# Optimization experiments

Measured on AMD Instinct MI355X. Metric: run time of the kernel, lower is better.

Reference implementation:

```python
import jax, jax.numpy as jnp
import numpy as np

N = 100000        # nodes
E = 1600000       # edges (avg degree 16)
IN, HID, OUT = 128, 128, 40
K = 3             # Chebyshev order
NUM_HID = 5       # hidden ChebConv layers between first and last


def setup_inputs() -> dict:
    key = jax.random.key(0)
    ks = jax.random.split(key, 8)
    s = 0.05
    return dict(
        features=jax.random.normal(ks[0], (N, IN), jnp.float32),
        src=jax.random.randint(ks[1], (E,), 0, N),
        dst=jax.random.randint(ks[2], (E,), 0, N),
        W0=jax.random.normal(ks[3], (K * IN, HID), jnp.float32) * s,
        b0=jnp.zeros((HID,), jnp.float32),
        Wh=jax.random.normal(ks[4], (NUM_HID, K * HID, HID), jnp.float32) * s,
        bh=jnp.zeros((NUM_HID, HID), jnp.float32),
        Wl=jax.random.normal(ks[5], (K * HID, OUT), jnp.float32) * s,
        bl=jnp.zeros((OUT,), jnp.float32),
    )


def _cheb_conv(X, src, dst, dinv, W, b):
    """One DGL ChebConv with lambda_max=2 (re_norm=1): relu(cat(X_0..X_{K-1}) @ W + b)."""
    def spmm(Y):  # A_hat @ Y = D^-1/2 A D^-1/2 Y via gather/segment-sum
        msg = (Y * dinv)[src]                                  # [E, d]
        return jax.ops.segment_sum(msg, dst, num_segments=N) * dinv

    X0 = X
    bases = [X0]
    X1 = -spmm(X0)                       # X_1 = -A_hat X  (re_norm - 1 == 0)
    bases.append(X1)
    for _ in range(2, K):
        X2 = -2.0 * spmm(X1) - X0        # X_t = -2 A_hat X_{t-1} - X_{t-2}
        bases.append(X2)
        X0, X1 = X1, X2
    Xt = jnp.concatenate(bases, axis=1)  # [N, K*d]
    return jax.nn.relu(Xt @ W + b)


def reference(features, src, dst, W0, b0, Wh, bh, Wl, bl):
    # symmetric normalization from in-degrees (clamped at 1), as in DGL ChebConv
    deg = jax.ops.segment_sum(jnp.ones((E,), jnp.float32), dst, num_segments=N)
    dinv = jnp.clip(deg, 1.0, None) ** -0.5
    dinv = dinv[:, None]                 # [N, 1]

    h = _cheb_conv(features, src, dst, dinv, W0, b0)
    for i in range(NUM_HID):             # dropout is identity in eval mode
        h = _cheb_conv(h, src, dst, dinv, Wh[i], bh[i])
    return _cheb_conv(h, src, dst, dinv, Wl, bl)
```

## Files before the change

### kernel.cpp

```cpp
#include <hip/hip_runtime.h>
#include <hip/hip_bf16.h>


#define NN 100000
#define EE 1600000
#define FF 128
#define NBK 1563
#define EPB 4096
#define CAP 3072

typedef __attribute__((ext_vector_type(8))) short short8_t;
typedef __attribute__((ext_vector_type(8))) _Float16 half8_t;
typedef __attribute__((ext_vector_type(4))) _Float16 half4_t;
typedef __attribute__((ext_vector_type(4))) float floatx4;
typedef __attribute__((ext_vector_type(4))) float accfrag;


__global__ __launch_bounds__(256) void bhist_kernel(const int* __restrict__ dst,
                                                    int* __restrict__ bcnt) {
    __shared__ int lh[NBK];
    int tid = threadIdx.x;
    for (int j = tid; j < NBK; j += 256) lh[j] = 0;
    __syncthreads();
    int e0 = blockIdx.x * EPB;
#pragma unroll
    for (int k = 0; k < EPB / 256; ++k) {
        int i = e0 + k * 256 + tid;
        if (i < EE) atomicAdd(&lh[dst[i] >> 6], 1);
    }
    __syncthreads();
    for (int j = tid; j < NBK; j += 256)
        if (lh[j] > 0) atomicAdd(&bcnt[j], lh[j]);
}

__global__ __launch_bounds__(256) void scan_p1_kernel(const int* __restrict__ cnt,
                                                      int* __restrict__ bsum, int n) {
    __shared__ int red[8];
    int i = blockIdx.x * 256 + threadIdx.x;
    int v = (i < n) ? cnt[i] : 0;
    for (int off = 32; off > 0; off >>= 1) v += __shfl_down(v, off, 64);
    int wv = threadIdx.x >> 6;
    if ((threadIdx.x & 63) == 0) red[wv] = v;
    __syncthreads();
    if (threadIdx.x == 0) bsum[blockIdx.x] = red[0] + red[1] + red[2] + red[3];
}

__global__ __launch_bounds__(1024) void scan_p2_kernel(int* __restrict__ bsum, int nb) {
    __shared__ int s[1024];
    int tid = threadIdx.x;
    int v = (tid < nb) ? bsum[tid] : 0;
    s[tid] = v;
    __syncthreads();
    for (int off = 1; off < 1024; off <<= 1) {
        int u = (tid >= off) ? s[tid - off] : 0;
        __syncthreads();
        s[tid] += u;
        __syncthreads();
    }
    if (tid < nb) bsum[tid] = s[tid] - v;
}

__global__ __launch_bounds__(256) void scan_p3_kernel(const int* __restrict__ cnt,
                                                      const int* __restrict__ bsum,
                                                      int* __restrict__ out_ptr, int n) {
    __shared__ int s[256];
    int tid = threadIdx.x;
    int i = blockIdx.x * 256 + tid;
    int v = (i < n) ? cnt[i] : 0;
    s[tid] = v;
    __syncthreads();
    for (int off = 1; off < 256; off <<= 1) {
        int u = (tid >= off) ? s[tid - off] : 0;
        __syncthreads();
        s[tid] += u;
        __syncthreads();
    }
    if (i < n) {
        int excl = bsum[blockIdx.x] + s[tid] - v;
        out_ptr[i] = excl;
        if (i == n - 1) out_ptr[n] = excl + v;
    }
}

__global__ __launch_bounds__(256) void bscatter_kernel(
    const int* __restrict__ src, const int* __restrict__ dst,
    const int* __restrict__ bptr, int* __restrict__ bfill, int* __restrict__ ebuf) {
    __shared__ int lh[NBK];
    __shared__ int lbase[NBK];
    int tid = threadIdx.x;
    for (int j = tid; j < NBK; j += 256) lh[j] = 0;
    __syncthreads();
    int e0 = blockIdx.x * EPB;
#pragma unroll
    for (int k = 0; k < EPB / 256; ++k) {
        int i = e0 + k * 256 + tid;
        if (i < EE) atomicAdd(&lh[dst[i] >> 6], 1);
    }
    __syncthreads();
    for (int j = tid; j < NBK; j += 256)
        if (lh[j] > 0) lbase[j] = atomicAdd(&bfill[j], lh[j]);
    __syncthreads();
    for (int j = tid; j < NBK; j += 256) lh[j] = 0;
    __syncthreads();
#pragma unroll
    for (int k = 0; k < EPB / 256; ++k) {
        int i = e0 + k * 256 + tid;
        if (i < EE) {
            int d = dst[i];
            int b = d >> 6;
            int off = atomicAdd(&lh[b], 1);
            ebuf[bptr[b] + lbase[b] + off] = (src[i] << 6) | (d & 63);
        }
    }
}

__global__ __launch_bounds__(256) void csr_build_kernel(
    const int* __restrict__ ebuf, const int* __restrict__ bptr,
    int* __restrict__ rowptr, int* __restrict__ colsrc,
    float* __restrict__ dinv, float* __restrict__ dinv2, float* __restrict__ sdeg) {
    __shared__ int pk[CAP];
    __shared__ int ob[CAP];
    __shared__ int cnt[64];
    __shared__ int sexcl[64];
    __shared__ int fill[64];

    int tid = threadIdx.x;
    int b = blockIdx.x;
    int start = bptr[b];
    int cb = bptr[b + 1] - start;
    if (cb > CAP) cb = CAP;

    if (tid < 64) { cnt[tid] = 0; fill[tid] = 0; }
    __syncthreads();

    for (int i = tid; i < cb; i += 256) {
        int v = ebuf[start + i];
        pk[i] = v;
        atomicAdd(&cnt[v & 63], 1);
    }
    __syncthreads();

    if (tid < 64) {
        int v = cnt[tid];
        int inc = v;
        for (int off = 1; off < 64; off <<= 1) {
            int u = __shfl_up(inc, off, 64);
            if (tid >= off) inc += u;
        }
        int excl = inc - v;
        sexcl[tid] = excl;
        int gnode = b * 64 + tid;
        if (gnode < NN) {
            rowptr[gnode] = start + excl;
            int d = v < 1 ? 1 : v;
            float fd = (float)d;
            dinv[gnode]  = 1.0f / sqrtf(fd);
            dinv2[gnode] = 1.0f / fd;
            sdeg[gnode]  = sqrtf(fd);
        }
    }
    if (b == 0 && tid == 0) rowptr[NN] = EE;
    __syncthreads();

    for (int i = tid; i < cb; i += 256) {
        int v = pk[i];
        int d = v & 63;
        int off = atomicAdd(&fill[d], 1);
        ob[sexcl[d] + off] = v >> 6;
    }
    __syncthreads();

    for (int i = tid; i < cb; i += 256) colsrc[start + i] = ob[i];
}


__global__ __launch_bounds__(256) void wprep_kernel(
    const float* __restrict__ W0, const float* __restrict__ Wh, const float* __restrict__ Wl,
    _Float16* __restrict__ Wh16)
{
    int idx = blockIdx.x * 256 + threadIdx.x;
    const int PER = 128 * 384;
    if (idx >= 7 * PER) return;
    int layer = idx / PER;
    int rem = idx - layer * PER;
    int ncol = rem / 384;
    int k = rem - ncol * 384;
    const float* W; int outc;
    if (layer == 0)      { W = W0; outc = 128; }
    else if (layer < 6)  { W = Wh + (size_t)(layer - 1) * 384 * 128; outc = 128; }
    else                 { W = Wl; outc = 40; }
    float v = (ncol < outc) ? W[(size_t)k * outc + ncol] : 0.f;
    Wh16[idx] = (_Float16)v;
}


__global__ __launch_bounds__(256) void fcvt_kernel(const float* __restrict__ in,
                                                   const float* __restrict__ dinv,
                                                   _Float16* __restrict__ out, int total4) {
    int i = blockIdx.x * 256 + threadIdx.x;
    if (i >= total4) return;
    int node = i >> 5;
    float dv = dinv[node];
    floatx4 v = *(const floatx4*)&in[i * 4];
    half4_t r = { (_Float16)(dv * v.x), (_Float16)(dv * v.y),
                  (_Float16)(dv * v.z), (_Float16)(dv * v.w) };
    *(half4_t*)&out[i * 4] = r;
}


__global__ __launch_bounds__(256) void spmm_h_kernel(
    _Float16* __restrict__ out, const _Float16* __restrict__ Xin,
    const _Float16* __restrict__ Xo, const float* __restrict__ dinv2,
    const int* __restrict__ rp, const int* __restrict__ cs,
    float alpha, float beta, int n)
{
    int slot = threadIdx.x >> 4;
    int lane = threadIdx.x & 15;
    int node = blockIdx.x * 16 + slot;
    if (node >= n) return;
    const half8_t* X8 = (const half8_t*)Xin;
    float acc[8] = { 0.f, 0.f, 0.f, 0.f, 0.f, 0.f, 0.f, 0.f };
    int s = rp[node], e = rp[node + 1];
    int cnt = e - s;
    int efull = s + (cnt & ~7);
    int i = s;
    for (; i < efull; i += 8) {
        int idx[8];
#pragma unroll
        for (int u = 0; u < 8; ++u) idx[u] = cs[i + u];
        half8_t x[8];
#pragma unroll
        for (int u = 0; u < 8; ++u) x[u] = X8[(size_t)idx[u] * 16 + lane];
#pragma unroll
        for (int u = 0; u < 8; ++u)
#pragma unroll
            for (int j = 0; j < 8; ++j) acc[j] += (float)x[u][j];
    }
    if (i < e) {
        int idx[8];
#pragma unroll
        for (int u = 0; u < 8; ++u) {
            int ii = i + u;
            idx[u] = cs[(ii < e) ? ii : (e - 1)];
        }
        half8_t x[8];
#pragma unroll
        for (int u = 0; u < 8; ++u) x[u] = X8[(size_t)idx[u] * 16 + lane];
#pragma unroll
        for (int u = 0; u < 8; ++u) {
            float m = (i + u < e) ? 1.0f : 0.0f;
#pragma unroll
            for (int j = 0; j < 8; ++j) acc[j] = fmaf(m, (float)x[u][j], acc[j]);
        }
    }
    float sc = alpha * dinv2[node];
    half8_t r;
    if (beta != 0.f) {
        half8_t o = ((const half8_t*)Xo)[(size_t)node * 16 + lane];
#pragma unroll
        for (int j = 0; j < 8; ++j) r[j] = (_Float16)(sc * acc[j] + beta * (float)o[j]);
    } else {
#pragma unroll
        for (int j = 0; j < 8; ++j) r[j] = (_Float16)(sc * acc[j]);
    }
    ((half8_t*)out)[(size_t)node * 16 + lane] = r;
}


template <int OUTC, int NT, bool HOUT>
__global__ __launch_bounds__(256, 4) void gemm_f16_kernel(
    void* __restrict__ outp, const _Float16* __restrict__ X0,
    const _Float16* __restrict__ X1, const _Float16* __restrict__ X2,
    const _Float16* __restrict__ Wh16, const float* __restrict__ bias,
    const float* __restrict__ sdeg, const float* __restrict__ dinv, int n)
{
    __shared__ _Float16 Ws[NT * 16][136];

    int tid = threadIdx.x;
    int lane = tid & 63;
    int wave = tid >> 6;
    int m15 = lane & 15;
    int quad = lane >> 4;
    int row0 = blockIdx.x * 128 + wave * 32;

    accfrag acc[2][NT];
#pragma unroll
    for (int mi = 0; mi < 2; ++mi)
#pragma unroll
        for (int nj = 0; nj < NT; ++nj) acc[mi][nj] = (accfrag){0.f, 0.f, 0.f, 0.f};

    int r0 = row0 + m15;
    int r1 = r0 + 16;
    size_t ro0 = (size_t)((r0 < n) ? r0 : 0) * 16;
    size_t ro1 = (size_t)((r1 < n) ? r1 : 0) * 16;

    const _Float16* srcs[3] = { X0, X1, X2 };

    for (int sb = 0; sb < 3; ++sb) {
        {
            const int VEC = NT * 256;
#pragma unroll
            for (int v0 = 0; v0 < VEC; v0 += 256) {
                int v = v0 + tid;
                int row = v >> 4;
                int c8 = (v & 15) * 8;
                *(half8_t*)&Ws[row][c8] =
                    *(const half8_t*)(Wh16 + (size_t)row * 384 + sb * 128 + c8);
            }
        }
        __syncthreads();

        const half8_t* Xp8 = (const half8_t*)srcs[sb];
#pragma unroll
        for (int kk = 0; kk < 4; ++kk) {
            int k0 = kk * 32 + quad * 8;
            half8_t a0 = Xp8[ro0 + kk * 4 + quad];
            half8_t a1 = Xp8[ro1 + kk * 4 + quad];
#pragma unroll
            for (int nj = 0; nj < NT; ++nj) {
                half8_t bfr = *(const half8_t*)&Ws[nj * 16 + m15][k0];
                acc[0][nj] = __builtin_amdgcn_mfma_f32_16x16x32_f16(a0, bfr, acc[0][nj], 0, 0, 0);
                acc[1][nj] = __builtin_amdgcn_mfma_f32_16x16x32_f16(a1, bfr, acc[1][nj], 0, 0, 0);
            }
        }
        __syncthreads();
    }

    float rs[2][4];
#pragma unroll
    for (int mi = 0; mi < 2; ++mi)
#pragma unroll
        for (int reg = 0; reg < 4; ++reg) {
            int gr = row0 + mi * 16 + quad * 4 + reg;
            int cg = (gr < n) ? gr : 0;
            rs[mi][reg] = HOUT ? dinv[cg] : sdeg[cg];
        }
#pragma unroll
    for (int nj = 0; nj < NT; ++nj) {
        int col = nj * 16 + m15;
        float bv = (col < OUTC) ? bias[col] : 0.f;
#pragma unroll
        for (int mi = 0; mi < 2; ++mi) {
#pragma unroll
            for (int reg = 0; reg < 4; ++reg) {
                int gr = row0 + mi * 16 + quad * 4 + reg;
                if (gr < n && col < OUTC) {
                    if (HOUT) {
                        float v = acc[mi][nj][reg] + rs[mi][reg] * bv;
                        v = v > 0.f ? v : 0.f;
                        ((_Float16*)outp)[(size_t)gr * OUTC + col] = (_Float16)v;
                    } else {
                        float v = rs[mi][reg] * acc[mi][nj][reg] + bv;
                        v = v > 0.f ? v : 0.f;
                        ((float*)outp)[(size_t)gr * OUTC + col] = v;
                    }
                }
            }
        }
    }
}


extern "C" void kernel_launch(void* const* d_in, const int* in_sizes, int n_in,
                              void* d_out, int out_size, void* d_ws, size_t ws_size,
                              hipStream_t stream) {
    const float* features = (const float*)d_in[0];
    const int*   src      = (const int*)d_in[1];
    const int*   dst      = (const int*)d_in[2];
    const float* W0       = (const float*)d_in[3];
    const float* b0       = (const float*)d_in[4];
    const float* Wh       = (const float*)d_in[5];
    const float* bh       = (const float*)d_in[6];
    const float* Wl       = (const float*)d_in[7];
    const float* bl       = (const float*)d_in[8];
    float* out = (float*)d_out;

    const int N = NN, E = EE;
    const int WTOT = 7 * 128 * 384;
    const int EB = (E + EPB - 1) / EPB;
    const int NB2 = (NBK + 255) / 256;

    char* ws = (char*)d_ws;
    size_t off = 0;
    auto alloc = [&](size_t bytes) -> void* {
        void* p = ws + off;
        off += (bytes + 511) & ~(size_t)511;
        return p;
    };
    int*      bcnt   = (int*)alloc((size_t)NBK * 4);
    int*      bfill  = (int*)alloc((size_t)NBK * 4);
    int*      bptr   = (int*)alloc((size_t)(NBK + 1) * 4);
    int*      bsum   = (int*)alloc((size_t)NB2 * 4);
    int*      rowptr = (int*)alloc((size_t)(N + 1) * 4);
    int*      ebuf   = (int*)alloc((size_t)E * 4);
    int*      colsrc = (int*)alloc((size_t)E * 4);
    float*    dinv   = (float*)alloc((size_t)N * 4);
    float*    dinv2  = (float*)alloc((size_t)N * 4);
    float*    sdeg   = (float*)alloc((size_t)N * 4);
    _Float16* Wh16   = (_Float16*)alloc((size_t)WTOT * 2);
    _Float16* XA     = (_Float16*)alloc((size_t)N * FF * 2);
    _Float16* XB     = (_Float16*)alloc((size_t)N * FF * 2);
    _Float16* B1     = (_Float16*)alloc((size_t)N * FF * 2);
    _Float16* B2     = (_Float16*)alloc((size_t)N * FF * 2);

    hipMemsetAsync(bcnt, 0, (size_t)NBK * 4, stream);
    hipMemsetAsync(bfill, 0, (size_t)NBK * 4, stream);
    bhist_kernel<<<EB, 256, 0, stream>>>(dst, bcnt);
    wprep_kernel<<<(WTOT + 255) / 256, 256, 0, stream>>>(W0, Wh, Wl, Wh16);
    scan_p1_kernel<<<NB2, 256, 0, stream>>>(bcnt, bsum, NBK);
    scan_p2_kernel<<<1, 1024, 0, stream>>>(bsum, NB2);
    scan_p3_kernel<<<NB2, 256, 0, stream>>>(bcnt, bsum, bptr, NBK);
    bscatter_kernel<<<EB, 256, 0, stream>>>(src, dst, bptr, bfill, ebuf);
    csr_build_kernel<<<NBK, 256, 0, stream>>>(ebuf, bptr, rowptr, colsrc, dinv, dinv2, sdeg);
    fcvt_kernel<<<(N * FF / 4 + 255) / 256, 256, 0, stream>>>(features, dinv, XA, N * FF / 4);

    const _Float16* cur = XA;
    _Float16* nxt = XB;
    int spmm_grid = (N + 15) / 16;
    int gemm_grid = (N + 127) / 128;

    for (int layer = 0; layer < 7; ++layer) {
        const float* b;
        bool last = (layer == 6);
        if (layer == 0)      { b = b0; }
        else if (layer < 6)  { b = bh + (layer - 1) * 128; }
        else                 { b = bl; }
        const _Float16* wl16 = Wh16 + (size_t)layer * 128 * 384;

        spmm_h_kernel<<<spmm_grid, 256, 0, stream>>>(B1, cur, cur, dinv2, rowptr, colsrc, -1.f, 0.f, N);
        spmm_h_kernel<<<spmm_grid, 256, 0, stream>>>(B2, B1, cur, dinv2, rowptr, colsrc, -2.f, -1.f, N);

        if (!last)
            gemm_f16_kernel<128, 8, true><<<gemm_grid, 256, 0, stream>>>(
                (void*)nxt, cur, B1, B2, wl16, b, sdeg, dinv, N);
        else
            gemm_f16_kernel<40, 3, false><<<gemm_grid, 256, 0, stream>>>(
                (void*)out, cur, B1, B2, wl16, b, sdeg, dinv, N);

        if (layer < 6) {
            const _Float16* newcur = nxt;
            nxt = (_Float16*)((nxt == XB) ? XA : XB);
            cur = newcur;
        }
    }
}
```

Before: 1.193 ms.

## Fuse second Chebyshev SpMM into GEMM kernel via shared-memory X2 tile

```diff
diff --git a/kernel.cpp b/kernel.cpp
--- a/kernel.cpp
+++ b/kernel.cpp
@@ -268,13 +268,17 @@
 
 
 template <int OUTC, int NT, bool HOUT>
-__global__ __launch_bounds__(256, 4) void gemm_f16_kernel(
-    void* __restrict__ outp, const _Float16* __restrict__ X0,
-    const _Float16* __restrict__ X1, const _Float16* __restrict__ X2,
+__global__ __launch_bounds__(256, 3) void cheb_fused_kernel(
+    void* __restrict__ outp,
+    const _Float16* __restrict__ X0,
+    const _Float16* __restrict__ X1,
     const _Float16* __restrict__ Wh16, const float* __restrict__ bias,
-    const float* __restrict__ sdeg, const float* __restrict__ dinv, int n)
+    const float* __restrict__ sdeg, const float* __restrict__ dinv,
+    const float* __restrict__ dinv2,
+    const int* __restrict__ rp, const int* __restrict__ cs, int n)
 {
-    __shared__ _Float16 Ws[NT * 16][136];
+    __shared__ _Float16 Ws[64][136];
+    __shared__ _Float16 X2s[128][136];
 
     int tid = threadIdx.x;
     int lane = tid & 63;
@@ -283,6 +287,133 @@
     int quad = lane >> 4;
     int row0 = blockIdx.x * 128 + wave * 32;
 
+    {
+        int lane16 = tid & 15;
+        int sid = (tid >> 4) & 3;
+        const half8_t* G8 = (const half8_t*)X1;
+        const half8_t* C8 = (const half8_t*)X0;
+#pragma unroll
+        for (int r = 0; r < 8; r += 2) {
+            int ln0 = wave * 32 + sid * 8 + r;
+            int ln1 = ln0 + 1;
+            int nd0 = blockIdx.x * 128 + ln0;
+            int nd1 = nd0 + 1;
+            float a0[8] = {0.f,0.f,0.f,0.f,0.f,0.f,0.f,0.f};
+            float a1[8] = {0.f,0.f,0.f,0.f,0.f,0.f,0.f,0.f};
+            int s0 = 0, e0 = 0, s1 = 0, e1 = 0;
+            if (nd0 < n) { s0 = rp[nd0]; e0 = rp[nd0 + 1]; }
+            if (nd1 < n) { s1 = rp[nd1]; e1 = rp[nd1 + 1]; }
+            int i0 = s0, i1 = s1;
+            int f0 = s0 + ((e0 - s0) & ~7);
+            int f1 = s1 + ((e1 - s1) & ~7);
+            while (i0 < f0 && i1 < f1) {
+                int ix0[8], ix1[8];
+#pragma unroll
+                for (int u = 0; u < 8; ++u) { ix0[u] = cs[i0 + u]; ix1[u] = cs[i1 + u]; }
+                half8_t x0[8], x1[8];
+#pragma unroll
+                for (int u = 0; u < 8; ++u) x0[u] = G8[(size_t)ix0[u] * 16 + lane16];
+#pragma unroll
+                for (int u = 0; u < 8; ++u) x1[u] = G8[(size_t)ix1[u] * 16 + lane16];
+#pragma unroll
+                for (int u = 0; u < 8; ++u)
+#pragma unroll
+                    for (int j = 0; j < 8; ++j) a0[j] += (float)x0[u][j];
+#pragma unroll
+                for (int u = 0; u < 8; ++u)
+#pragma unroll
+                    for (int j = 0; j < 8; ++j) a1[j] += (float)x1[u][j];
+                i0 += 8; i1 += 8;
+            }
+            for (; i0 < f0; i0 += 8) {
+                int ix[8];
+#pragma unroll
+                for (int u = 0; u < 8; ++u) ix[u] = cs[i0 + u];
+                half8_t x[8];
+#pragma unroll
+                for (int u = 0; u < 8; ++u) x[u] = G8[(size_t)ix[u] * 16 + lane16];
+#pragma unroll
+                for (int u = 0; u < 8; ++u)
+#pragma unroll
+                    for (int j = 0; j < 8; ++j) a0[j] += (float)x[u][j];
+            }
+            for (; i1 < f1; i1 += 8) {
+                int ix[8];
+#pragma unroll
+                for (int u = 0; u < 8; ++u) ix[u] = cs[i1 + u];
+                half8_t x[8];
+#pragma unroll
+                for (int u = 0; u < 8; ++u) x[u] = G8[(size_t)ix[u] * 16 + lane16];
+#pragma unroll
+                for (int u = 0; u < 8; ++u)
+#pragma unroll
+                    for (int j = 0; j < 8; ++j) a1[j] += (float)x[u][j];
+            }
+            if (i0 < e0) {
+                int ix[8];
+#pragma unroll
+                for (int u = 0; u < 8; ++u) {
+                    int ii = i0 + u;
+                    ix[u] = cs[(ii < e0) ? ii : (e0 - 1)];
+                }
+                half8_t x[8];
+#pragma unroll
+                for (int u = 0; u < 8; ++u) x[u] = G8[(size_t)ix[u] * 16 + lane16];
+#pragma unroll
+                for (int u = 0; u < 8; ++u) {
+                    float m = (i0 + u < e0) ? 1.0f : 0.0f;
+#pragma unroll
+                    for (int j = 0; j < 8; ++j) a0[j] = fmaf(m, (float)x[u][j], a0[j]);
+                }
+            }
+            if (i1 < e1) {
+                int ix[8];
+#pragma unroll
+                for (int u = 0; u < 8; ++u) {
+                    int ii = i1 + u;
+                    ix[u] = cs[(ii < e1) ? ii : (e1 - 1)];
+                }
+                half8_t x[8];
+#pragma unroll
+                for (int u = 0; u < 8; ++u) x[u] = G8[(size_t)ix[u] * 16 + lane16];
+#pragma unroll
+                for (int u = 0; u < 8; ++u) {
+                    float m = (i1 + u < e1) ? 1.0f : 0.0f;
+#pragma unroll
+                    for (int j = 0; j < 8; ++j) a1[j] = fmaf(m, (float)x[u][j], a1[j]);
+                }
+            }
+            {
+                half8_t w0;
+                if (nd0 < n) {
+                    float sc = -2.0f * dinv2[nd0];
+                    half8_t c = C8[(size_t)nd0 * 16 + lane16];
+#pragma unroll
+                    for (int j = 0; j < 8; ++j) w0[j] = (_Float16)(sc * a0[j] - (float)c[j]);
+                } else {
+#pragma unroll
+                    for (int j = 0; j < 8; ++j) w0[j] = (_Float16)0.f;
+                }
+                *(half8_t*)&X2s[ln0][lane16 * 8] = w0;
+            }
+            {
+                half8_t w1;
+                if (nd1 < n) {
+                    float sc = -2.0f * dinv2[nd1];
+                    half8_t c = C8[(size_t)nd1 * 16 + lane16];
+#pragma unroll
+                    for (int j = 0; j < 8; ++j) w1[j] = (_Float16)(sc * a1[j] - (float)c[j]);
+                } else {
+#pragma unroll
+                    for (int j = 0; j < 8; ++j) w1[j] = (_Float16)0.f;
+                }
+                *(half8_t*)&X2s[ln1][lane16 * 8] = w1;
+            }
+        }
+    }
+
+    constexpr int NH = (NT + 3) / 4;
+
     accfrag acc[2][NT];
 #pragma unroll
     for (int mi = 0; mi < 2; ++mi)
@@ -294,36 +425,57 @@
     size_t ro0 = (size_t)((r0 < n) ? r0 : 0) * 16;
     size_t ro1 = (size_t)((r1 < n) ? r1 : 0) * 16;
 
-    const _Float16* srcs[3] = { X0, X1, X2 };
-
+#pragma unroll
     for (int sb = 0; sb < 3; ++sb) {
-        {
-            const int VEC = NT * 256;
-#pragma unroll
-            for (int v0 = 0; v0 < VEC; v0 += 256) {
+        half8_t aa0[4], aa1[4];
+        if (sb < 2) {
+            const half8_t* Xp8 = (const half8_t*)(sb == 0 ? X0 : X1);
+#pragma unroll
+            for (int kk = 0; kk < 4; ++kk) {
+                aa0[kk] = Xp8[ro0 + kk * 4 + quad];
+                aa1[kk] = Xp8[ro1 + kk * 4 + quad];
+            }
+        } else {
+            int lr0 = wave * 32 + m15;
+#pragma unroll
+            for (int kk = 0; kk < 4; ++kk) {
+                aa0[kk] = *(const half8_t*)&X2s[lr0][(kk * 4 + quad) * 8];
+                aa1[kk] = *(const half8_t*)&X2s[lr0 + 16][(kk * 4 + quad) * 8];
+            }
+        }
+#pragma unroll
+        for (int h = 0; h < NH; ++h) {
+            constexpr int R16 = NT * 16;
+            int rowsH = R16 - h * 64; if (rowsH > 64) rowsH = 64;
+            int vec = rowsH * 16;
+            for (int v0 = 0; v0 < vec; v0 += 256) {
                 int v = v0 + tid;
-                int row = v >> 4;
-                int c8 = (v & 15) * 8;
-                *(half8_t*)&Ws[row][c8] =
-                    *(const half8_t*)(Wh16 + (size_t)row * 384 + sb * 128 + c8);
-            }
-        }
-        __syncthreads();
-
-        const half8_t* Xp8 = (const half8_t*)srcs[sb];
-#pragma unroll
-        for (int kk = 0; kk < 4; ++kk) {
-            int k0 = kk * 32 + quad * 8;
-            half8_t a0 = Xp8[ro0 + kk * 4 + quad];
-            half8_t a1 = Xp8[ro1 + kk * 4 + quad];
-#pragma unroll
-            for (int nj = 0; nj < NT; ++nj) {
-                half8_t bfr = *(const half8_t*)&Ws[nj * 16 + m15][k0];
-                acc[0][nj] = __builtin_amdgcn_mfma_f32_16x16x32_f16(a0, bfr, acc[0][nj], 0, 0, 0);
-                acc[1][nj] = __builtin_amdgcn_mfma_f32_16x16x32_f16(a1, bfr, acc[1][nj], 0, 0, 0);
-            }
-        }
-        __syncthreads();
+                if (v < vec) {
+                    int rL = v >> 4;
+                    int c8 = (v & 15) * 8;
+                    *(half8_t*)&Ws[rL][c8] =
+                        *(const half8_t*)(Wh16 + (size_t)(h * 64 + rL) * 384 + sb * 128 + c8);
+                }
+            }
+            __syncthreads();
+            constexpr int NJC0 = (NT > 4) ? 4 : NT;
+            const int njc = (h == 0) ? NJC0 : (NT - 4 > 4 ? 4 : NT - 4);
+#pragma unroll
+            for (int kk = 0; kk < 4; ++kk) {
+                int k0 = kk * 32 + quad * 8;
+#pragma unroll
+                for (int nj = 0; nj < NJC0; ++nj) {
+                    if (nj < njc) {
+                        half8_t bfr = *(const half8_t*)&Ws[nj * 16 + m15][k0];
+                        acc[0][h * 4 + nj] = __builtin_amdgcn_mfma_f32_16x16x32_f16(
+                            aa0[kk], bfr, acc[0][h * 4 + nj], 0, 0, 0);
+                        acc[1][h * 4 + nj] = __builtin_amdgcn_mfma_f32_16x16x32_f16(
+                            aa1[kk], bfr, acc[1][h * 4 + nj], 0, 0, 0);
+                    }
+                }
+            }
+            __syncthreads();
+        }
     }
 
     float rs[2][4];
@@ -401,7 +553,6 @@
     _Float16* XA     = (_Float16*)alloc((size_t)N * FF * 2);
     _Float16* XB     = (_Float16*)alloc((size_t)N * FF * 2);
     _Float16* B1     = (_Float16*)alloc((size_t)N * FF * 2);
-    _Float16* B2     = (_Float16*)alloc((size_t)N * FF * 2);
 
     hipMemsetAsync(bcnt, 0, (size_t)NBK * 4, stream);
     hipMemsetAsync(bfill, 0, (size_t)NBK * 4, stream);
@@ -428,14 +579,13 @@
         const _Float16* wl16 = Wh16 + (size_t)layer * 128 * 384;
 
         spmm_h_kernel<<<spmm_grid, 256, 0, stream>>>(B1, cur, cur, dinv2, rowptr, colsrc, -1.f, 0.f, N);
-        spmm_h_kernel<<<spmm_grid, 256, 0, stream>>>(B2, B1, cur, dinv2, rowptr, colsrc, -2.f, -1.f, N);
 
         if (!last)
-            gemm_f16_kernel<128, 8, true><<<gemm_grid, 256, 0, stream>>>(
-                (void*)nxt, cur, B1, B2, wl16, b, sdeg, dinv, N);
+            cheb_fused_kernel<128, 8, true><<<gemm_grid, 256, 0, stream>>>(
+                (void*)nxt, cur, B1, wl16, b, sdeg, dinv, dinv2, rowptr, colsrc, N);
         else
-            gemm_f16_kernel<40, 3, false><<<gemm_grid, 256, 0, stream>>>(
-                (void*)out, cur, B1, B2, wl16, b, sdeg, dinv, N);
+            cheb_fused_kernel<40, 3, false><<<gemm_grid, 256, 0, stream>>>(
+                (void*)out, cur, B1, wl16, b, sdeg, dinv, dinv2, rowptr, colsrc, N);
 
         if (layer < 6) {
             const _Float16* newcur = nxt;
```

New measurement: 1.396 ms. 17.0% more time.
